# Kernel tuning notes

Measured on AMD Instinct MI355X. Metric: run time of the kernel, lower is better.

The kernel has to match this reference:

```python
import jax, jax.numpy as jnp
import numpy as np

G = [1, 1, 1]          # Clifford signature Cl(3,0) -> I = 8 blades
N_FREE = 20            # EPEngine n_free
DT = 0.1               # EPEngine dt
IN_DIM, HIDDEN_DIM, OUT_DIM = 64, 512, 64
BATCH = 8192
I_BLADES = 2 ** len(G)


def _cayley(g):
    """Dense blade multiplication table C[a, b, a^b] = sign for Cl(g)."""
    n = len(g)
    I = 2 ** n
    C = np.zeros((I, I, I), dtype=np.float32)
    for a in range(I):
        for b in range(I):
            # reordering sign: for each vector in b, count vectors of a above it
            s = 0
            for i in range(n):
                if (b >> i) & 1:
                    s += bin(a >> (i + 1)).count('1')
            sign = (-1.0) ** s
            # metric contraction on shared basis vectors
            common = a & b
            for i in range(n):
                if (common >> i) & 1:
                    sign *= g[i]
            C[a, b, a ^ b] = sign
    return C

CAYLEY = jnp.asarray(_cayley(G))  # (I, I, I), sparse signed table


def geometric_product(x, W):
    # x: (B, M, I), W: (H, M, I) -> (B, H, I); contract shared dim M and blades via Cayley
    xc = jnp.einsum('bma,ack->bmck', x, CAYLEY)   # (B, M, I, I), cheap (I=8)
    return jnp.einsum('bmck,hmc->bhk', xc, W)


def setup_inputs() -> dict:
    key = jax.random.key(0)
    k1, k2, k3 = jax.random.split(key, 3)
    x_mv = jax.random.normal(k1, (BATCH, IN_DIM, I_BLADES), dtype=jnp.float32)
    W_in = jax.random.normal(k2, (HIDDEN_DIM, IN_DIM, I_BLADES), dtype=jnp.float32) * 0.1
    W_out = jax.random.normal(k3, (OUT_DIM, HIDDEN_DIM, I_BLADES), dtype=jnp.float32) * 0.1
    return {"x_mv": x_mv, "W_in": W_in, "W_out": W_out}


def reference(x_mv, W_in, W_out):
    # Energy E(h) = 0.5*||h||^2 - <h, Wx>  =>  dE/dh = h - Wx
    Wx = geometric_product(x_mv, W_in)                    # (B, H, I), input term is h-independent
    B, H, I = Wx.shape
    h0 = jnp.zeros((B, H, I), dtype=x_mv.dtype)

    def step(h, _):
        # free-phase relaxation: h <- h - dt * dE/dh
        return h + DT * (Wx - h), None

    h_free, _ = jax.lax.scan(step, h0, None, length=N_FREE)
    pred_mv = geometric_product(h_free, W_out)            # (B, O, I)
    # task_type == 'invariant': scalar part, flattened to (B, out_dim)
    return pred_mv[..., 0].reshape(B, -1)
```

## Files before the change

kernel.cpp:

```cpp
#include <hip/hip_runtime.h>
#include <hip/hip_bf16.h>

#define BATCH 8192
#define MDIM  64
#define HDIM  512
#define ODIM  64
#define IB    8
#define K2    512
#define S_PAD 520

typedef float  f32x4  __attribute__((ext_vector_type(4)));
typedef __bf16 bf16x8 __attribute__((ext_vector_type(8)));

__host__ __device__ constexpr float cay(int a, int b) {
    int s = 0;
    for (int i = 0; i < 3; ++i)
        if ((b >> i) & 1) {
            int x = a >> (i + 1);
            s += (x & 1) + ((x >> 1) & 1) + ((x >> 2) & 1);
        }
    return (s & 1) ? -1.0f : 1.0f;
}

struct CoefT { float c[8][8]; };
constexpr CoefT make_coef() {
    CoefT t{};
    for (int p = 0; p < 8; ++p)
        for (int q = 0; q < 8; ++q)
            t.c[p][q] = cay(p, q) * cay(p ^ q, p ^ q);
    return t;
}
constexpr CoefT COEF = make_coef();

__device__ __forceinline__ unsigned short f2bf(float f) {
    __hip_bfloat16 h = __float2bfloat16(f);
    return __builtin_bit_cast(unsigned short, h);
}

__global__ __launch_bounds__(256) void k_precompute_mfma(
        const float* __restrict__ Win,
        const float* __restrict__ Wout,
        unsigned short* __restrict__ Abf,
        float alpha) {
    __shared__ unsigned short At[32 * S_PAD];
    __shared__ unsigned short Bt[32 * S_PAD];
    __shared__ float Tlds[32 * 32];

    const int tid = threadIdx.x;
    const int wv  = tid >> 6;
    const int l   = tid & 63;
    const int mg  = blockIdx.x & 15;
    const int og  = blockIdx.x >> 4;

    {
        const int fr  = l & 31;
        const int hh  = l >> 5;
        const int o_l = fr >> 3, c = fr & 7;
        for (int it = 0; it < 8; ++it) {
            const int h0 = wv * 128 + it * 16 + hh * 8;
            float a[8], b[8];
            #pragma unroll
            for (int j = 0; j < 8; ++j)
                a[j] = Win[(h0 + j) * 512 + mg * 32 + fr];
            #pragma unroll
            for (int j = 0; j < 8; ++j)
                b[j] = Wout[(og * 4 + o_l) * (HDIM * IB) + (h0 + j) * IB + c];
            unsigned short ua[8], ub[8];
            #pragma unroll
            for (int j = 0; j < 8; ++j) { ua[j] = f2bf(a[j]); ub[j] = f2bf(b[j]); }
            *reinterpret_cast<uint4*>(&At[fr * S_PAD + h0]) = *reinterpret_cast<uint4*>(ua);
            *reinterpret_cast<uint4*>(&Bt[fr * S_PAD + h0]) = *reinterpret_cast<uint4*>(ub);
        }
    }
    __syncthreads();

    const int lr = l & 15, lq = l >> 4;
    const int wr = wv & 1, wc = wv >> 1;
    const unsigned short* arow = &At[(wr * 16 + lr) * S_PAD];
    const unsigned short* brow = &Bt[(wc * 16 + lr) * S_PAD];

    f32x4 acc = {0.0f, 0.0f, 0.0f, 0.0f};
    #pragma unroll
    for (int ks = 0; ks < 16; ++ks) {
        bf16x8 af = *reinterpret_cast<const bf16x8*>(arow + ks * 32 + lq * 8);
        bf16x8 bf = *reinterpret_cast<const bf16x8*>(brow + ks * 32 + lq * 8);
        acc = __builtin_amdgcn_mfma_f32_16x16x32_bf16(af, bf, acc, 0, 0, 0);
    }

    #pragma unroll
    for (int r = 0; r < 4; ++r)
        Tlds[(wr * 16 + lq * 4 + r) * 32 + wc * 16 + lr] = acc[r];
    __syncthreads();

    if (tid < 128) {
        const int o_l = tid >> 5;
        const int m_l = (tid >> 3) & 3;
        const int p   = tid & 7;
        float s = 0.0f;
        #pragma unroll
        for (int q = 0; q < 8; ++q)
            s += COEF.c[p][q] * Tlds[(m_l * 8 + q) * 32 + o_l * 8 + (p ^ q)];
        Abf[(og * 4 + o_l) * K2 + (mg * 4 + m_l) * 8 + p] = f2bf(alpha * s);
    }
}

__global__ __launch_bounds__(256) void k_main(
        const float* __restrict__ X,
        const unsigned short* __restrict__ Abf,
        float* __restrict__ Out) {
    __shared__ unsigned short xs[16 * K2];

    const int tid = threadIdx.x;
    const int b0  = blockIdx.x * 16;

    const int wave = tid >> 6;
    const int l    = tid & 63;
    const int lr   = l & 15;
    const int lq   = l >> 4;

    const unsigned short* bbase = Abf + (wave * 16 + lr) * K2 + lq * 8;
    bf16x8 bfr[16];
    #pragma unroll
    for (int ks = 0; ks < 16; ++ks)
        bfr[ks] = *reinterpret_cast<const bf16x8*>(bbase + ks * 32);

    #pragma unroll
    for (int t = 0; t < 4; ++t) {
        int idx  = t * 256 + tid;
        int ks   = idx >> 6;
        int lane = idx & 63;
        int row  = lane & 15;
        int col0 = ks * 32 + (lane >> 4) * 8;
        const float* src = X + (long)(b0 + row) * K2 + col0;
        float4 v0 = *reinterpret_cast<const float4*>(src);
        float4 v1 = *reinterpret_cast<const float4*>(src + 4);
        ushort4 u0, u1;
        u0.x = f2bf(v0.x); u0.y = f2bf(v0.y); u0.z = f2bf(v0.z); u0.w = f2bf(v0.w);
        u1.x = f2bf(v1.x); u1.y = f2bf(v1.y); u1.z = f2bf(v1.z); u1.w = f2bf(v1.w);
        unsigned short* dst = &xs[ks * 512 + lane * 8];
        reinterpret_cast<ushort4*>(dst)[0] = u0;
        reinterpret_cast<ushort4*>(dst)[1] = u1;
    }
    __syncthreads();

    f32x4 acc = {0.0f, 0.0f, 0.0f, 0.0f};
    #pragma unroll
    for (int ks = 0; ks < 16; ++ks) {
        bf16x8 af = *reinterpret_cast<const bf16x8*>(&xs[ks * 512 + l * 8]);
        acc = __builtin_amdgcn_mfma_f32_16x16x32_bf16(af, bfr[ks], acc, 0, 0, 0);
    }

    float* o = Out + (long)(b0 + lq * 4) * ODIM + wave * 16 + lr;
    #pragma unroll
    for (int r = 0; r < 4; ++r) o[r * ODIM] = acc[r];
}

extern "C" void kernel_launch(void* const* d_in, const int* in_sizes, int n_in,
                              void* d_out, int out_size, void* d_ws, size_t ws_size,
                              hipStream_t stream) {
    const float* x    = (const float*)d_in[0];
    const float* Win  = (const float*)d_in[1];
    const float* Wout = (const float*)d_in[2];
    float* out = (float*)d_out;

    unsigned short* Abf = (unsigned short*)d_ws;

    const float alpha = 0.8784233454094307f;

    k_precompute_mfma<<<256, 256, 0, stream>>>(Win, Wout, Abf, alpha);
    k_main           <<<512, 256, 0, stream>>>(x, Abf, out);
}
```

Baseline: 74.25 us.

## Fuse weight precompute and main GEMM into one cooperative kernel

```diff
diff --git a/kernel.cpp b/kernel.cpp
--- a/kernel.cpp
+++ b/kernel.cpp
@@ -1,5 +1,6 @@
 #include <hip/hip_runtime.h>
 #include <hip/hip_bf16.h>
+#include <hip/hip_cooperative_groups.h>
 
 #define BATCH 8192
 #define MDIM  64
@@ -35,6 +36,126 @@
 __device__ __forceinline__ unsigned short f2bf(float f) {
     __hip_bfloat16 h = __float2bfloat16(f);
     return __builtin_bit_cast(unsigned short, h);
+}
+
+__global__ __launch_bounds__(512) void k_fused(
+        const float* __restrict__ X,
+        const float* __restrict__ Win,
+        const float* __restrict__ Wout,
+        unsigned short* __restrict__ Abf,
+        float* __restrict__ Out,
+        float alpha) {
+    __shared__ unsigned short At[32 * S_PAD];
+    __shared__ unsigned short Bt[32 * S_PAD];
+    __shared__ float Tlds[32 * 32];
+    __shared__ unsigned short xs[2 * 16 * 512];
+
+    const int tid = threadIdx.x;
+    const int b0  = blockIdx.x * 32;
+    const int mg  = blockIdx.x & 15;
+    const int og  = blockIdx.x >> 4;
+
+    if (tid < 256) {
+        const int wv  = tid >> 6;
+        const int l   = tid & 63;
+        const int fr  = l & 31;
+        const int hh  = l >> 5;
+        const int o_l = fr >> 3, c = fr & 7;
+        for (int it = 0; it < 8; ++it) {
+            const int h0 = wv * 128 + it * 16 + hh * 8;
+            float a[8], b[8];
+            #pragma unroll
+            for (int j = 0; j < 8; ++j)
+                a[j] = Win[(h0 + j) * 512 + mg * 32 + fr];
+            #pragma unroll
+            for (int j = 0; j < 8; ++j)
+                b[j] = Wout[(og * 4 + o_l) * (HDIM * IB) + (h0 + j) * IB + c];
+            unsigned short ua[8], ub[8];
+            #pragma unroll
+            for (int j = 0; j < 8; ++j) { ua[j] = f2bf(a[j]); ub[j] = f2bf(b[j]); }
+            *reinterpret_cast<uint4*>(&At[fr * S_PAD + h0]) = *reinterpret_cast<uint4*>(ua);
+            *reinterpret_cast<uint4*>(&Bt[fr * S_PAD + h0]) = *reinterpret_cast<uint4*>(ub);
+        }
+    } else {
+        const int t = tid - 256;
+        #pragma unroll
+        for (int i = 0; i < 8; ++i) {
+            int idx  = i * 256 + t;
+            int rt2  = idx >> 10;
+            int ks   = (idx >> 6) & 15;
+            int lane = idx & 63;
+            int row  = rt2 * 16 + (lane & 15);
+            int col0 = ks * 32 + (lane >> 4) * 8;
+            const float* src = X + (long)(b0 + row) * K2 + col0;
+            float4 v0 = *reinterpret_cast<const float4*>(src);
+            float4 v1 = *reinterpret_cast<const float4*>(src + 4);
+            ushort4 u0, u1;
+            u0.x = f2bf(v0.x); u0.y = f2bf(v0.y); u0.z = f2bf(v0.z); u0.w = f2bf(v0.w);
+            u1.x = f2bf(v1.x); u1.y = f2bf(v1.y); u1.z = f2bf(v1.z); u1.w = f2bf(v1.w);
+            unsigned short* dst = &xs[rt2 * 8192 + ks * 512 + lane * 8];
+            reinterpret_cast<ushort4*>(dst)[0] = u0;
+            reinterpret_cast<ushort4*>(dst)[1] = u1;
+        }
+    }
+    __syncthreads();
+
+    if (tid < 256) {
+        const int wv = tid >> 6;
+        const int l  = tid & 63;
+        const int lr = l & 15, lq = l >> 4;
+        const int wr = wv & 1, wc = wv >> 1;
+        const unsigned short* arow = &At[(wr * 16 + lr) * S_PAD];
+        const unsigned short* brow = &Bt[(wc * 16 + lr) * S_PAD];
+
+        f32x4 acc = {0.0f, 0.0f, 0.0f, 0.0f};
+        #pragma unroll
+        for (int ks = 0; ks < 16; ++ks) {
+            bf16x8 af = *reinterpret_cast<const bf16x8*>(arow + ks * 32 + lq * 8);
+            bf16x8 bf = *reinterpret_cast<const bf16x8*>(brow + ks * 32 + lq * 8);
+            acc = __builtin_amdgcn_mfma_f32_16x16x32_bf16(af, bf, acc, 0, 0, 0);
+        }
+        #pragma unroll
+        for (int r = 0; r < 4; ++r)
+            Tlds[(wr * 16 + lq * 4 + r) * 32 + wc * 16 + lr] = acc[r];
+    }
+    __syncthreads();
+
+    if (tid < 128) {
+        const int o_l = tid >> 5;
+        const int m_l = (tid >> 3) & 3;
+        const int p   = tid & 7;
+        float s = 0.0f;
+        #pragma unroll
+        for (int q = 0; q < 8; ++q)
+            s += COEF.c[p][q] * Tlds[(m_l * 8 + q) * 32 + o_l * 8 + (p ^ q)];
+        Abf[(og * 4 + o_l) * K2 + (mg * 4 + m_l) * 8 + p] = f2bf(alpha * s);
+    }
+
+    cooperative_groups::this_grid().sync();
+
+    {
+        const int w  = tid >> 6;
+        const int l  = tid & 63;
+        const int lr = l & 15, lq = l >> 4;
+        const int ot = w & 3, rt = w >> 2;
+
+        const unsigned short* bbase = Abf + (ot * 16 + lr) * K2 + lq * 8;
+        bf16x8 bfr[16];
+        #pragma unroll
+        for (int ks = 0; ks < 16; ++ks)
+            bfr[ks] = *reinterpret_cast<const bf16x8*>(bbase + ks * 32);
+
+        f32x4 acc = {0.0f, 0.0f, 0.0f, 0.0f};
+        #pragma unroll
+        for (int ks = 0; ks < 16; ++ks) {
+            bf16x8 af = *reinterpret_cast<const bf16x8*>(&xs[rt * 8192 + ks * 512 + l * 8]);
+            acc = __builtin_amdgcn_mfma_f32_16x16x32_bf16(af, bfr[ks], acc, 0, 0, 0);
+        }
+
+        float* o = Out + (long)(b0 + rt * 16 + lq * 4) * ODIM + ot * 16 + lr;
+        #pragma unroll
+        for (int r = 0; r < 4; ++r) o[r * ODIM] = acc[r];
+    }
 }
 
 __global__ __launch_bounds__(256) void k_precompute_mfma(
@@ -165,8 +286,15 @@
 
     unsigned short* Abf = (unsigned short*)d_ws;
 
-    const float alpha = 0.8784233454094307f;
-
-    k_precompute_mfma<<<256, 256, 0, stream>>>(Win, Wout, Abf, alpha);
-    k_main           <<<512, 256, 0, stream>>>(x, Abf, out);
-}
+    float alpha = 0.8784233454094307f;
+
+    void* args[] = {(void*)&x, (void*)&Win, (void*)&Wout,
+                    (void*)&Abf, (void*)&out, (void*)&alpha};
+    hipError_t e = hipLaunchCooperativeKernel((const void*)k_fused,
+                                              dim3(256), dim3(512),
+                                              args, 0, stream);
+    if (e != hipSuccess) {
+        k_precompute_mfma<<<256, 256, 0, stream>>>(Win, Wout, Abf, alpha);
+        k_main           <<<512, 256, 0, stream>>>(x, Abf, out);
+    }
+}
```

Result: slower. 107.8 us (+45.1%).
